# Kernel optimization log

Hardware: AMD Instinct MI355X
Metric: run time of the kernel (lower is better)

## Reference

```python
import jax, jax.numpy as jnp
import numpy as np

N = 512
C = 256


def _edge_feat(n, s, v, W, b):
    # e_ij = n_i * n_j * s_ij  (elementwise triple product), shape (N, N, C)
    e = jnp.einsum('nc,mc,nmc->nmc', n, n, s)
    # Linear applied per-edge: torch y = x @ W.T + b with W (out, in)
    e = jnp.einsum('nmc,dc->nmd', e, W) + b
    return e * v


def setup_inputs() -> dict:
    key = jax.random.key(0)
    ks = jax.random.split(key, 9)
    scale = 1.0 / np.sqrt(C)
    return {
        'n': jax.random.normal(ks[0], (N, C), dtype=jnp.float32),
        's': jax.random.normal(ks[1], (N, N, C), dtype=jnp.float32),
        'v': jax.random.normal(ks[2], (N, N, C), dtype=jnp.float32),
        'Wq': jax.random.normal(ks[3], (C, C), dtype=jnp.float32) * scale,
        'bq': jax.random.normal(ks[4], (C,), dtype=jnp.float32) * scale,
        'Wk': jax.random.normal(ks[5], (C, C), dtype=jnp.float32) * scale,
        'bk': jax.random.normal(ks[6], (C,), dtype=jnp.float32) * scale,
        'Wv': jax.random.normal(ks[7], (C, C), dtype=jnp.float32) * scale,
        'bv': jax.random.normal(ks[8], (C,), dtype=jnp.float32) * scale,
    }


def reference(n, s, v, Wq, bq, Wk, bk, Wv, bv):
    q = _edge_feat(n, s, v, Wq, bq)   # (N, N, C)
    k = _edge_feat(n, s, v, Wk, bk)   # (N, N, C)
    ve = _edge_feat(n, s, v, Wv, bv)  # (N, N, C)
    # channel-reduced attention scores per edge pair: (N, N)
    scores = jnp.einsum('nmc,nmc->nm', q, k) / jnp.sqrt(jnp.float32(C))
    attn = jax.nn.softmax(scores, axis=-1)
    x = jnp.einsum('nm,nmc->nc', attn, ve)  # (N, C)
    x = x + n
    norms = jnp.linalg.norm(x, axis=1, keepdims=True)
    return x / norms
```

## Files before the change

### kernel.cpp

```cpp
#include <hip/hip_runtime.h>

#define N 512
#define C 256

#define TJB 32
#define JT  8
#define DT  4

#define TJ 16

__device__ __forceinline__ float f4c(const float4 v, const int i)
{
    return i == 0 ? v.x : i == 1 ? v.y : i == 2 ? v.z : v.w;
}

__global__ __launch_bounds__(256) void k_transpose(
    const float* __restrict__ Wq, const float* __restrict__ Wk,
    const float* __restrict__ Wv, float* __restrict__ wt_base)
{
    __shared__ float tile[32][33];
    const float* W = blockIdx.z == 0 ? Wq : blockIdx.z == 1 ? Wk : Wv;
    float* Wt = wt_base + (size_t)blockIdx.z * C * C;
    const int tx  = threadIdx.x & 31;
    const int ty0 = threadIdx.x >> 5;
    const int bx = blockIdx.x * 32;
    const int by = blockIdx.y * 32;
    #pragma unroll
    for (int r = 0; r < 4; ++r)
        tile[ty0 + r * 8][tx] = W[(size_t)(by + ty0 + r * 8) * C + bx + tx];
    __syncthreads();
    #pragma unroll
    for (int r = 0; r < 4; ++r)
        Wt[(size_t)(bx + ty0 + r * 8) * C + by + tx] = tile[tx][ty0 + r * 8];
}

template<bool WRITE_VE>
__global__ __launch_bounds__(256, 2) void k_edge(
    const float* __restrict__ n_g, const float* __restrict__ s_g,
    const float* __restrict__ v_g,
    const float* __restrict__ wqt, const float* __restrict__ bq,
    const float* __restrict__ wkt, const float* __restrict__ bk,
    const float* __restrict__ wvt, const float* __restrict__ bv,
    float* __restrict__ scores, float* __restrict__ veW)
{
    __shared__ float e_lds[TJB][C];
    const int i  = blockIdx.x;
    const int jb = blockIdx.y * TJB;
    const int t  = threadIdx.x;
    const int dg = t & 63;
    const int jg = t >> 6;
    const int jl = jg * JT;

    const float ni = n_g[i * C + t];
    #pragma unroll 4
    for (int j = 0; j < TJB; ++j) {
        const int jj = jb + j;
        e_lds[j][t] = ni * n_g[jj * C + t] * s_g[((size_t)i * N + jj) * C + t];
    }
    __syncthreads();

    float aq[DT][JT], ak[DT][JT], av[DT][JT];
    #pragma unroll
    for (int dr = 0; dr < DT; ++dr)
        #pragma unroll
        for (int jr = 0; jr < JT; ++jr) { aq[dr][jr] = 0.f; ak[dr][jr] = 0.f; av[dr][jr] = 0.f; }

    const float4* wq4 = (const float4*)wqt;
    const float4* wk4 = (const float4*)wkt;
    const float4* wv4 = (const float4*)wvt;

    for (int c4 = 0; c4 < C / 4; ++c4) {
        float4 ev[JT];
        #pragma unroll
        for (int jr = 0; jr < JT; ++jr)
            ev[jr] = *(const float4*)&e_lds[jl + jr][c4 * 4];

        #pragma unroll
        for (int cs = 0; cs < 4; ++cs) {
            const int c = c4 * 4 + cs;
            const float4 wq = wq4[c * 64 + dg];
            const float4 wk = wk4[c * 64 + dg];
            const float4 wv = wv4[c * 64 + dg];
            #pragma unroll
            for (int jr = 0; jr < JT; ++jr) {
                const float e = f4c(ev[jr], cs);
                #pragma unroll
                for (int dr = 0; dr < DT; ++dr) {
                    aq[dr][jr] = fmaf(f4c(wq, dr), e, aq[dr][jr]);
                    ak[dr][jr] = fmaf(f4c(wk, dr), e, ak[dr][jr]);
                    av[dr][jr] = fmaf(f4c(wv, dr), e, av[dr][jr]);
                }
            }
        }
    }

    const float4 bq4 = *(const float4*)&bq[4 * dg];
    const float4 bk4 = *(const float4*)&bk[4 * dg];
    const float4 bv4 = *(const float4*)&bv[4 * dg];

    #pragma unroll
    for (int jr = 0; jr < JT; ++jr) {
        const int jj = jb + jl + jr;
        const size_t eoff = ((size_t)i * N + jj) * C + 4 * dg;
        const float4 vv = *(const float4*)&v_g[eoff];
        float r = 0.f;
        float4 veo;
        #pragma unroll
        for (int dr = 0; dr < DT; ++dr) {
            const float qh = aq[dr][jr] + f4c(bq4, dr);
            const float kh = ak[dr][jr] + f4c(bk4, dr);
            const float vd = f4c(vv, dr);
            r += qh * kh * vd * vd;
            const float vo = (av[dr][jr] + f4c(bv4, dr)) * vd;
            if (dr == 0) veo.x = vo; else if (dr == 1) veo.y = vo;
            else if (dr == 2) veo.z = vo; else veo.w = vo;
        }
        if constexpr (WRITE_VE)
            *(float4*)&veW[eoff] = veo;
        #pragma unroll
        for (int off = 32; off > 0; off >>= 1)
            r += __shfl_down(r, off, 64);
        if (dg == 0)
            scores[(size_t)i * N + jj] = r * (1.0f / 16.0f);
    }
}

__global__ __launch_bounds__(256) void k_softmax(float* __restrict__ buf)
{
    __shared__ float red[4];
    const int i = blockIdx.x;
    const int t = threadIdx.x;
    const int lane = t & 63, wid = t >> 6;

    const float a = buf[(size_t)i * N + t];
    const float b = buf[(size_t)i * N + t + 256];
    float m = fmaxf(a, b);
    #pragma unroll
    for (int off = 32; off > 0; off >>= 1)
        m = fmaxf(m, __shfl_xor(m, off, 64));
    if (lane == 0) red[wid] = m;
    __syncthreads();
    m = fmaxf(fmaxf(red[0], red[1]), fmaxf(red[2], red[3]));

    const float ea = __expf(a - m), eb = __expf(b - m);
    float ssum = ea + eb;
    #pragma unroll
    for (int off = 32; off > 0; off >>= 1)
        ssum += __shfl_xor(ssum, off, 64);
    __syncthreads();
    if (lane == 0) red[wid] = ssum;
    __syncthreads();
    const float inv = 1.0f / (red[0] + red[1] + red[2] + red[3]);
    buf[(size_t)i * N + t]       = ea * inv;
    buf[(size_t)i * N + t + 256] = eb * inv;
}

__global__ __launch_bounds__(256) void k_gather(
    const float* __restrict__ n_g, const float* __restrict__ veW,
    const float* __restrict__ attn, float* __restrict__ out)
{
    __shared__ float att_s[N];
    __shared__ float part[4];
    const int i = blockIdx.x;
    const int t = threadIdx.x;
    const int lane = t & 63, wid = t >> 6;

    att_s[t]       = attn[(size_t)i * N + t];
    att_s[t + 256] = attn[(size_t)i * N + t + 256];
    __syncthreads();

    const float* base = veW + (size_t)i * N * C + t;
    float xacc = 0.0f;
    for (int j = 0; j < N; j += 8) {
        const float p0 = base[(size_t)(j + 0) * C];
        const float p1 = base[(size_t)(j + 1) * C];
        const float p2 = base[(size_t)(j + 2) * C];
        const float p3 = base[(size_t)(j + 3) * C];
        const float p4 = base[(size_t)(j + 4) * C];
        const float p5 = base[(size_t)(j + 5) * C];
        const float p6 = base[(size_t)(j + 6) * C];
        const float p7 = base[(size_t)(j + 7) * C];
        xacc += att_s[j+0]*p0 + att_s[j+1]*p1 + att_s[j+2]*p2 + att_s[j+3]*p3
              + att_s[j+4]*p4 + att_s[j+5]*p5 + att_s[j+6]*p6 + att_s[j+7]*p7;
    }

    const float x = xacc + n_g[i * C + t];
    float sq = x * x;
    #pragma unroll
    for (int off = 32; off > 0; off >>= 1)
        sq += __shfl_xor(sq, off, 64);
    if (lane == 0) part[wid] = sq;
    __syncthreads();
    const float nrm = sqrtf(part[0] + part[1] + part[2] + part[3]);
    out[i * C + t] = x / nrm;
}

__global__ __launch_bounds__(256) void k_scores_old(
    const float* __restrict__ n_g, const float* __restrict__ s_g,
    const float* __restrict__ v_g,
    const float* __restrict__ Wq, const float* __restrict__ bq,
    const float* __restrict__ Wk, const float* __restrict__ bk,
    float* __restrict__ scores)
{
    __shared__ float e_lds[TJ][C];
    __shared__ float part[4][TJ];
    const int i  = blockIdx.x;
    const int jb = blockIdx.y * TJ;
    const int t  = threadIdx.x;
    const int lane = t & 63, wid = t >> 6;

    const float ni = n_g[i * C + t];
    #pragma unroll
    for (int j = 0; j < TJ; ++j) {
        const int jj = jb + j;
        e_lds[j][t] = ni * n_g[jj * C + t] * s_g[((size_t)i * N + jj) * C + t];
    }
    __syncthreads();

    float accq[TJ], acck[TJ];
    const float bqd = bq[t], bkd = bk[t];
    #pragma unroll
    for (int j = 0; j < TJ; ++j) { accq[j] = bqd; acck[j] = bkd; }

    const float4* wq4 = (const float4*)(Wq + (size_t)t * C);
    const float4* wk4 = (const float4*)(Wk + (size_t)t * C);
    for (int c4 = 0; c4 < C / 4; ++c4) {
        const float4 wq = wq4[c4];
        const float4 wk = wk4[c4];
        #pragma unroll
        for (int j = 0; j < TJ; ++j) {
            const float4 ev = *(const float4*)&e_lds[j][c4 * 4];
            accq[j] += wq.x*ev.x + wq.y*ev.y + wq.z*ev.z + wq.w*ev.w;
            acck[j] += wk.x*ev.x + wk.y*ev.y + wk.z*ev.z + wk.w*ev.w;
        }
    }

    #pragma unroll
    for (int j = 0; j < TJ; ++j) {
        const int jj = jb + j;
        const float vv = v_g[((size_t)i * N + jj) * C + t];
        float r = accq[j] * acck[j] * vv * vv;
        #pragma unroll
        for (int off = 32; off > 0; off >>= 1)
            r += __shfl_down(r, off, 64);
        if (lane == 0) part[wid][j] = r;
    }
    __syncthreads();
    if (t < TJ) {
        const float ssum = part[0][t] + part[1][t] + part[2][t] + part[3][t];
        scores[(size_t)i * N + jb + t] = ssum * (1.0f / 16.0f);
    }
}

__global__ __launch_bounds__(256) void k_out(
    const float* __restrict__ n_g, const float* __restrict__ s_g,
    const float* __restrict__ v_g,
    const float* __restrict__ Wv, const float* __restrict__ bv,
    const float* __restrict__ attn, float* __restrict__ out)
{
    __shared__ float e_lds[TJ][C];
    __shared__ float part[4];
    const int i = blockIdx.x;
    const int t = threadIdx.x;
    const int lane = t & 63, wid = t >> 6;

    const float ni  = n_g[i * C + t];
    const float bvd = bv[t];
    const float4* wv4 = (const float4*)(Wv + (size_t)t * C);
    float xacc = 0.0f;

    for (int jt = 0; jt < N / TJ; ++jt) {
        const int jb = jt * TJ;
        __syncthreads();
        #pragma unroll
        for (int j = 0; j < TJ; ++j) {
            const int jj = jb + j;
            e_lds[j][t] = ni * n_g[jj * C + t] * s_g[((size_t)i * N + jj) * C + t];
        }
        __syncthreads();

        float accv[TJ];
        #pragma unroll
        for (int j = 0; j < TJ; ++j) accv[j] = bvd;

        float4 vn = wv4[0];
        for (int c4 = 0; c4 < C / 4; ++c4) {
            const float4 wv = vn;
            if (c4 + 1 < C / 4) vn = wv4[c4 + 1];
            #pragma unroll
            for (int j = 0; j < TJ; ++j) {
                const float4 ev = *(const float4*)&e_lds[j][c4 * 4];
                accv[j] += wv.x*ev.x + wv.y*ev.y + wv.z*ev.z + wv.w*ev.w;
            }
        }
        #pragma unroll
        for (int j = 0; j < TJ; ++j) {
            const int jj = jb + j;
            const float a  = attn[(size_t)i * N + jj];
            const float vd = v_g[((size_t)i * N + jj) * C + t];
            xacc += a * accv[j] * vd;
        }
    }

    const float x = xacc + ni;
    float sq = x * x;
    #pragma unroll
    for (int off = 32; off > 0; off >>= 1)
        sq += __shfl_xor(sq, off, 64);
    if (lane == 0) part[wid] = sq;
    __syncthreads();
    const float nrm = sqrtf(part[0] + part[1] + part[2] + part[3]);
    out[i * C + t] = x / nrm;
}

extern "C" void kernel_launch(void* const* d_in, const int* in_sizes, int n_in,
                              void* d_out, int out_size, void* d_ws, size_t ws_size,
                              hipStream_t stream)
{
    const float* n_g = (const float*)d_in[0];
    const float* s_g = (const float*)d_in[1];
    const float* v_g = (const float*)d_in[2];
    const float* Wq  = (const float*)d_in[3];
    const float* bq  = (const float*)d_in[4];
    const float* Wk  = (const float*)d_in[5];
    const float* bk  = (const float*)d_in[6];
    const float* Wv  = (const float*)d_in[7];
    const float* bv  = (const float*)d_in[8];
    float* out = (float*)d_out;

    const size_t score_bytes = (size_t)N * N * sizeof(float);
    const size_t ve_bytes    = (size_t)N * N * C * sizeof(float);
    const size_t wt_bytes    = (size_t)3 * C * C * sizeof(float);

    float* scores = (float*)d_ws;

    if (ws_size >= score_bytes + ve_bytes + wt_bytes) {
        float* veW = (float*)((char*)d_ws + score_bytes);
        float* wt  = (float*)((char*)d_ws + score_bytes + ve_bytes);
        float* wqt = wt;
        float* wkt = wt + (size_t)C * C;
        float* wvt = wt + (size_t)2 * C * C;

        k_transpose<<<dim3(C / 32, C / 32, 3), 256, 0, stream>>>(Wq, Wk, Wv, wt);
        k_edge<true><<<dim3(N, N / TJB), 256, 0, stream>>>(
            n_g, s_g, v_g, wqt, bq, wkt, bk, wvt, bv, scores, veW);
        k_softmax<<<N, 256, 0, stream>>>(scores);
        k_gather <<<N, 256, 0, stream>>>(n_g, veW, scores, out);
    } else if (ws_size >= score_bytes + wt_bytes) {
        float* wt  = (float*)((char*)d_ws + score_bytes);
        float* wqt = wt;
        float* wkt = wt + (size_t)C * C;
        float* wvt = wt + (size_t)2 * C * C;

        k_transpose<<<dim3(C / 32, C / 32, 3), 256, 0, stream>>>(Wq, Wk, Wv, wt);
        k_edge<false><<<dim3(N, N / TJB), 256, 0, stream>>>(
            n_g, s_g, v_g, wqt, bq, wkt, bk, wvt, bv, scores, nullptr);
        k_softmax<<<N, 256, 0, stream>>>(scores);
        k_out    <<<N, 256, 0, stream>>>(n_g, s_g, v_g, Wv, bv, scores, out);
    } else {
        k_scores_old<<<dim3(N, N / TJ), 256, 0, stream>>>(
            n_g, s_g, v_g, Wq, bq, Wk, bk, scores);
        k_softmax<<<N, 256, 0, stream>>>(scores);
        k_out    <<<N, 256, 0, stream>>>(n_g, s_g, v_g, Wv, bv, scores, out);
    }
}
```

Baseline: 1.831 ms.

## Retile edge projection to 2 outputs x 16 edges with double-buffered weight loads

The edge kernel now gives each thread 2 output channels and 16 edges instead of 4 channels and 8 edges. Each LDS e-value is reused over fewer channels, but weight traffic per FMA drops. Weight loads are software double-buffered across c4 steps, and V weights are loaded only when ve is written. Because a 128-thread row group now spans two wavefronts, score reduction goes through a small LDS partial buffer and a second sync. Dropping the occupancy hint in launch_bounds lets the register count grow, which risks fewer resident waves.

```diff
diff --git a/kernel.cpp b/kernel.cpp
--- a/kernel.cpp
+++ b/kernel.cpp
@@ -4,8 +4,8 @@
 #define C 256
 
 #define TJB 32
-#define JT  8
-#define DT  4
+#define JT  16
+#define DT  2
 
 #define TJ 16
 
@@ -35,7 +35,7 @@
 }
 
 template<bool WRITE_VE>
-__global__ __launch_bounds__(256, 2) void k_edge(
+__global__ __launch_bounds__(256) void k_edge(
     const float* __restrict__ n_g, const float* __restrict__ s_g,
     const float* __restrict__ v_g,
     const float* __restrict__ wqt, const float* __restrict__ bq,
@@ -44,18 +44,21 @@
     float* __restrict__ scores, float* __restrict__ veW)
 {
     __shared__ float e_lds[TJB][C];
+    __shared__ float part[4][JT];
     const int i  = blockIdx.x;
     const int jb = blockIdx.y * TJB;
     const int t  = threadIdx.x;
-    const int dg = t & 63;
-    const int jg = t >> 6;
+    const int dg = t & 127;
+    const int jg = t >> 7;
     const int jl = jg * JT;
-
-    const float ni = n_g[i * C + t];
+    const int wv = t >> 6;
+    const int lane = t & 63;
+
+    const float nic = n_g[i * C + t];
     #pragma unroll 4
     for (int j = 0; j < TJB; ++j) {
         const int jj = jb + j;
-        e_lds[j][t] = ni * n_g[jj * C + t] * s_g[((size_t)i * N + jj) * C + t];
+        e_lds[j][t] = nic * n_g[jj * C + t] * s_g[((size_t)i * N + jj) * C + t];
     }
     __syncthreads();
 
@@ -65,63 +68,79 @@
         #pragma unroll
         for (int jr = 0; jr < JT; ++jr) { aq[dr][jr] = 0.f; ak[dr][jr] = 0.f; av[dr][jr] = 0.f; }
 
-    const float4* wq4 = (const float4*)wqt;
-    const float4* wk4 = (const float4*)wkt;
-    const float4* wv4 = (const float4*)wvt;
-
-    for (int c4 = 0; c4 < C / 4; ++c4) {
-        float4 ev[JT];
-        #pragma unroll
-        for (int jr = 0; jr < JT; ++jr)
-            ev[jr] = *(const float4*)&e_lds[jl + jr][c4 * 4];
-
+    const float2* wq2 = (const float2*)wqt;
+    const float2* wk2 = (const float2*)wkt;
+    const float2* wv2 = (const float2*)wvt;
+
+    float2 qA[4], kA[4], vA[4], qB[4], kB[4], vB[4];
+
+    auto loadw = [&](float2 (&q)[4], float2 (&k)[4], float2 (&v)[4], int c4) {
+        const int c0 = c4 * 4;
         #pragma unroll
         for (int cs = 0; cs < 4; ++cs) {
-            const int c = c4 * 4 + cs;
-            const float4 wq = wq4[c * 64 + dg];
-            const float4 wk = wk4[c * 64 + dg];
-            const float4 wv = wv4[c * 64 + dg];
+            q[cs] = wq2[(c0 + cs) * 128 + dg];
+            k[cs] = wk2[(c0 + cs) * 128 + dg];
+            if constexpr (WRITE_VE) v[cs] = wv2[(c0 + cs) * 128 + dg];
+        }
+    };
+    auto comp = [&](const float2 (&q)[4], const float2 (&k)[4], const float2 (&v)[4], int c4) {
+        #pragma unroll
+        for (int jr = 0; jr < JT; ++jr) {
+            const float4 ev = *(const float4*)&e_lds[jl + jr][c4 * 4];
             #pragma unroll
-            for (int jr = 0; jr < JT; ++jr) {
-                const float e = f4c(ev[jr], cs);
-                #pragma unroll
-                for (int dr = 0; dr < DT; ++dr) {
-                    aq[dr][jr] = fmaf(f4c(wq, dr), e, aq[dr][jr]);
-                    ak[dr][jr] = fmaf(f4c(wk, dr), e, ak[dr][jr]);
-                    av[dr][jr] = fmaf(f4c(wv, dr), e, av[dr][jr]);
+            for (int cs = 0; cs < 4; ++cs) {
+                const float e = f4c(ev, cs);
+                aq[0][jr] = fmaf(q[cs].x, e, aq[0][jr]);
+                aq[1][jr] = fmaf(q[cs].y, e, aq[1][jr]);
+                ak[0][jr] = fmaf(k[cs].x, e, ak[0][jr]);
+                ak[1][jr] = fmaf(k[cs].y, e, ak[1][jr]);
+                if constexpr (WRITE_VE) {
+                    av[0][jr] = fmaf(v[cs].x, e, av[0][jr]);
+                    av[1][jr] = fmaf(v[cs].y, e, av[1][jr]);
                 }
             }
         }
-    }
-
-    const float4 bq4 = *(const float4*)&bq[4 * dg];
-    const float4 bk4 = *(const float4*)&bk[4 * dg];
-    const float4 bv4 = *(const float4*)&bv[4 * dg];
+    };
+
+    loadw(qA, kA, vA, 0);
+    for (int c8 = 0; c8 < C / 8; ++c8) {
+        const int c4a = 2 * c8, c4b = c4a + 1;
+        loadw(qB, kB, vB, c4b);
+        comp (qA, kA, vA, c4a);
+        const int nxt = (c4b + 1 < C / 4) ? c4b + 1 : C / 4 - 1;
+        loadw(qA, kA, vA, nxt);
+        comp (qB, kB, vB, c4b);
+    }
+
+    const float2 bq2 = *(const float2*)&bq[2 * dg];
+    const float2 bk2 = *(const float2*)&bk[2 * dg];
+    float2 bv2;
+    if constexpr (WRITE_VE) bv2 = *(const float2*)&bv[2 * dg];
 
     #pragma unroll
     for (int jr = 0; jr < JT; ++jr) {
         const int jj = jb + jl + jr;
-        const size_t eoff = ((size_t)i * N + jj) * C + 4 * dg;
-        const float4 vv = *(const float4*)&v_g[eoff];
-        float r = 0.f;
-        float4 veo;
-        #pragma unroll
-        for (int dr = 0; dr < DT; ++dr) {
-            const float qh = aq[dr][jr] + f4c(bq4, dr);
-            const float kh = ak[dr][jr] + f4c(bk4, dr);
-            const float vd = f4c(vv, dr);
-            r += qh * kh * vd * vd;
-            const float vo = (av[dr][jr] + f4c(bv4, dr)) * vd;
-            if (dr == 0) veo.x = vo; else if (dr == 1) veo.y = vo;
-            else if (dr == 2) veo.z = vo; else veo.w = vo;
-        }
-        if constexpr (WRITE_VE)
-            *(float4*)&veW[eoff] = veo;
+        const size_t eoff = ((size_t)i * N + jj) * C + 2 * dg;
+        const float2 vv = *(const float2*)&v_g[eoff];
+        const float qh0 = aq[0][jr] + bq2.x, qh1 = aq[1][jr] + bq2.y;
+        const float kh0 = ak[0][jr] + bk2.x, kh1 = ak[1][jr] + bk2.y;
+        float r = qh0 * kh0 * vv.x * vv.x + qh1 * kh1 * vv.y * vv.y;
+        if constexpr (WRITE_VE) {
+            float2 veo;
+            veo.x = (av[0][jr] + bv2.x) * vv.x;
+            veo.y = (av[1][jr] + bv2.y) * vv.y;
+            *(float2*)&veW[eoff] = veo;
+        }
         #pragma unroll
         for (int off = 32; off > 0; off >>= 1)
             r += __shfl_down(r, off, 64);
-        if (dg == 0)
-            scores[(size_t)i * N + jj] = r * (1.0f / 16.0f);
+        if (lane == 0) part[wv][jr] = r;
+    }
+    __syncthreads();
+    if (t < 2 * JT) {
+        const int g = t >> 4, jr = t & 15;
+        const float ssum = part[2 * g][jr] + part[2 * g + 1][jr];
+        scores[(size_t)i * N + jb + g * JT + jr] = ssum * (1.0f / 16.0f);
     }
 }
 
```

Result: slower. 2.633 ms (+43.8%).
